# Kernel optimization log

Measured on AMD Instinct MI355X. Metric: run time of the kernel, lower is better.

Reference implementation:

```python
import jax, jax.numpy as jnp
import numpy as np

IN_F = 2048
OUT_F = 2048
BS = 64  # block_size
NIB = IN_F // BS   # 32 in-blocks
NOB = OUT_F // BS  # 32 out-blocks


def setup_inputs() -> dict:
    key = jax.random.key(0)
    k_x, k_s1, k_s2, k_m = jax.random.split(key, 4)
    bound = 1.0 / np.sqrt(BS)
    x = jax.random.normal(k_x, (4, 4096, IN_F), dtype=jnp.float32)
    stage1 = jax.random.uniform(k_s1, (NIB * BS, BS), minval=-bound, maxval=bound, dtype=jnp.float32)
    stage2 = jax.random.uniform(k_s2, (NOB * BS, BS), minval=-bound, maxval=bound, dtype=jnp.float32)
    mix_w = jax.random.normal(k_m, (NOB * BS, NIB * BS), dtype=jnp.float32) / np.sqrt(IN_F)
    return {"x": x, "stage1": stage1, "stage2": stage2, "mix_w": mix_w}


def _blockdiag(x, weight, num_blocks):
    # x: [..., num_blocks*BS]; weight: [num_blocks*BS, BS] viewed as [g, c, d]
    shape = x.shape[:-1]
    xg = x.reshape(-1, num_blocks, BS)
    w = weight.reshape(num_blocks, BS, BS)
    y = jnp.einsum('ngc,gcd->ngd', xg, w)
    return y.reshape(*shape, num_blocks * BS)


def _shuffle(x):
    # interpret last dim as [BS, NIB], transpose to [NIB, BS]
    shape = x.shape[:-1]
    return x.reshape(-1, BS, NIB).transpose(0, 2, 1).reshape(*shape, NIB * BS)


def reference(x, stage1, stage2, mix_w):
    h = _blockdiag(x, stage1, NIB)          # [B,S,IN_F]
    h = _shuffle(h)                          # [B,S,IN_F]
    h = jnp.einsum('bsi,oi->bso', h, mix_w)  # dense mix, no bias
    return _blockdiag(h, stage2, NOB)        # [B,S,OUT_F]
```

## Files before the change

### kernel.cpp

```cpp
#include <hip/hip_runtime.h>
#include <stdint.h>

#define IN_F 2048
#define OUT_F 2048
#define MTOK 16384

typedef __attribute__((ext_vector_type(8))) __bf16 bf16x8;
typedef __attribute__((ext_vector_type(4))) float f32x4;
typedef __attribute__((ext_vector_type(4))) unsigned short us4;
typedef __attribute__((ext_vector_type(8))) unsigned short us8;

typedef const __attribute__((address_space(1))) void g_void;
typedef __attribute__((address_space(3))) void l_void;

__device__ __forceinline__ void async16(void* lds, const void* g) {
    __builtin_amdgcn_global_load_lds((g_void*)(uintptr_t)g, (l_void*)(uintptr_t)lds, 16, 0, 0);
}

__device__ __forceinline__ unsigned short f2bf(float x) {
    union { float f; uint32_t u; } v; v.f = x;
    uint32_t r = v.u + 0x7fffu + ((v.u >> 16) & 1u);
    return (unsigned short)(r >> 16);
}

__device__ __forceinline__ bf16x8 f8_to_bf8(const float* __restrict__ p) {
    float4 a = *(const float4*)p;
    float4 b = *(const float4*)(p + 4);
    union { us8 u; bf16x8 h; } r;
    r.u[0] = f2bf(a.x); r.u[1] = f2bf(a.y); r.u[2] = f2bf(a.z); r.u[3] = f2bf(a.w);
    r.u[4] = f2bf(b.x); r.u[5] = f2bf(b.y); r.u[6] = f2bf(b.z); r.u[7] = f2bf(b.w);
    return r.h;
}

__global__ void k_prep(const float* __restrict__ W,
                       const float* __restrict__ s1, const float* __restrict__ s2,
                       unsigned short* __restrict__ Bp,
                       unsigned short* __restrict__ W1T, unsigned short* __restrict__ W2T) {
    __shared__ float buf[64 * 65];
    const int t = threadIdx.x;
    if (blockIdx.x < 2048) {
        const float* src = W + (size_t)blockIdx.x * IN_F;
#pragma unroll
        for (int q = 0; q < 2; ++q) {
            int id4 = q * 256 + t;
            float4 v = *(const float4*)(src + id4 * 4);
            int i = id4 * 4;
            int b = i + (i >> 5);
            buf[b] = v.x; buf[b + 1] = v.y; buf[b + 2] = v.z; buf[b + 3] = v.w;
        }
        __syncthreads();
        unsigned short* dst = Bp + (size_t)blockIdx.x * IN_F;
#pragma unroll
        for (int q = 0; q < 8; ++q) {
            int j = q * 256 + t;
            int i = ((j & 31) << 6) | (j >> 5);
            dst[j] = f2bf(buf[i + (i >> 5)]);
        }
    } else {
        const int b = blockIdx.x - 2048;
        const float* src = (b < 32 ? s1 : s2) + (size_t)(b & 31) * 4096;
        unsigned short* dst = (b < 32 ? W1T : W2T) + (size_t)(b & 31) * 4096;
#pragma unroll
        for (int q = 0; q < 16; ++q) {
            int id = q * 256 + t;
            buf[(id >> 6) * 65 + (id & 63)] = src[id];
        }
        __syncthreads();
#pragma unroll
        for (int q = 0; q < 16; ++q) {
            int id = q * 256 + t;
            int d = id >> 6, c = id & 63;
            dst[id] = f2bf(buf[c * 65 + d]);
        }
    }
}

#define HS_LD 72
__global__ __launch_bounds__(256, 4) void k_stage1(
    const float* __restrict__ X, const unsigned short* __restrict__ W1T,
    unsigned short* __restrict__ H) {
    __shared__ unsigned short Hs[128 * HS_LD];
    const int t = threadIdx.x;
    const int lane = t & 63, wave = t >> 6;
    const int quad = lane >> 4, l16 = lane & 15;
    const int m0 = blockIdx.x * 128;
    const int g = blockIdx.y;

    const unsigned short* Wg = W1T + g * 4096;
    bf16x8 wf[4][2];
#pragma unroll
    for (int j = 0; j < 4; ++j)
#pragma unroll
        for (int ks = 0; ks < 2; ++ks)
            wf[j][ks] = *(const bf16x8*)(Wg + (j * 16 + l16) * 64 + ks * 32 + quad * 8);

    bf16x8 af[2][2];
#pragma unroll
    for (int i = 0; i < 2; ++i)
#pragma unroll
        for (int ks = 0; ks < 2; ++ks)
            af[i][ks] = f8_to_bf8(X + (size_t)(m0 + wave * 32 + i * 16 + l16) * IN_F
                                    + g * 64 + ks * 32 + quad * 8);

    f32x4 acc[2][4];
#pragma unroll
    for (int i = 0; i < 2; ++i)
#pragma unroll
        for (int j = 0; j < 4; ++j) acc[i][j] = (f32x4)0.f;

#pragma unroll
    for (int ks = 0; ks < 2; ++ks)
#pragma unroll
        for (int i = 0; i < 2; ++i)
#pragma unroll
            for (int j = 0; j < 4; ++j)
                acc[i][j] = __builtin_amdgcn_mfma_f32_16x16x32_bf16(af[i][ks], wf[j][ks], acc[i][j], 0, 0, 0);

#pragma unroll
    for (int i = 0; i < 2; ++i)
#pragma unroll
        for (int j = 0; j < 4; ++j)
#pragma unroll
            for (int r = 0; r < 4; ++r)
                Hs[(wave * 32 + i * 16 + quad * 4 + r) * HS_LD + j * 16 + l16] = f2bf(acc[i][j][r]);
    __syncthreads();
#pragma unroll
    for (int p = 0; p < 4; ++p) {
        int id = p * 256 + t;
        int r = id >> 3, c = id & 7;
        us8 v = *(const us8*)(Hs + r * HS_LD + c * 8);
        *(us8*)(H + (size_t)(m0 + r) * IN_F + g * 64 + c * 8) = v;
    }
}

__global__ __launch_bounds__(256, 2) void k_mix_gemm(
    const unsigned short* __restrict__ A, const unsigned short* __restrict__ B,
    const unsigned short* __restrict__ W2T, float* __restrict__ C) {
    __shared__ unsigned short smem[16384];
    unsigned short* As = smem;
    unsigned short* Bs = smem + 8192;
    const int t = threadIdx.x;
    const int lane = t & 63, wave = t >> 6;
    const int quad = lane >> 4, l16 = lane & 15;
    const int mw = wave & 1, nw = wave >> 1;
    const int lin = blockIdx.y * 128 + blockIdx.x;
    const int m0 = (lin >> 4) * 128;
    const int n0 = (lin & 15) * 128;
    const int rr = t >> 3, chunk = t & 7;
    const int gsw = (chunk ^ (rr & 7)) * 8;
    const int lsw = l16 & 7;

    f32x4 acc[4][4];
#pragma unroll
    for (int i = 0; i < 4; ++i)
#pragma unroll
        for (int j = 0; j < 4; ++j) acc[i][j] = (f32x4)0.f;

    for (int kb = 0; kb < IN_F; kb += 64) {
#pragma unroll
        for (int q = 0; q < 4; ++q) {
            int r = q * 32 + rr;
            async16((char*)As + (size_t)(q * 4096 + t * 16),
                    A + (size_t)(m0 + r) * IN_F + kb + gsw);
            async16((char*)Bs + (size_t)(q * 4096 + t * 16),
                    B + (size_t)(n0 + r) * IN_F + kb + gsw);
        }
        __syncthreads();
#pragma unroll
        for (int ks = 0; ks < 2; ++ks) {
            bf16x8 af[4], bfr[4];
#pragma unroll
            for (int i = 0; i < 4; ++i)
                af[i] = *(const bf16x8*)(As + (mw * 64 + i * 16 + l16) * 64
                                            + (((ks * 4 + quad) ^ lsw) * 8));
#pragma unroll
            for (int j = 0; j < 4; ++j)
                bfr[j] = *(const bf16x8*)(Bs + (nw * 64 + j * 16 + l16) * 64
                                             + (((ks * 4 + quad) ^ lsw) * 8));
#pragma unroll
            for (int i = 0; i < 4; ++i)
#pragma unroll
                for (int j = 0; j < 4; ++j)
                    acc[i][j] = __builtin_amdgcn_mfma_f32_16x16x32_bf16(af[i], bfr[j], acc[i][j], 0, 0, 0);
        }
        __syncthreads();
    }

    unsigned short* P = smem + wave * 4096;
#pragma unroll
    for (int i = 0; i < 4; ++i)
#pragma unroll
        for (int j = 0; j < 4; ++j) {
            int cc = j * 2 + (l16 >> 3);
            int ci = l16 & 7;
#pragma unroll
            for (int r = 0; r < 4; ++r) {
                int pr = i * 16 + quad * 4 + r;
                P[pr * 64 + ((cc ^ (pr & 7)) * 8) + ci] = f2bf(acc[i][j][r]);
            }
        }

    const int g = (n0 >> 6) + nw;
    const unsigned short* W2g = W2T + g * 4096;
    bf16x8 wb[4][2];
#pragma unroll
    for (int j = 0; j < 4; ++j)
#pragma unroll
        for (int ks = 0; ks < 2; ++ks)
            wb[j][ks] = *(const bf16x8*)(W2g + (j * 16 + l16) * 64 + ks * 32 + quad * 8);

#pragma unroll
    for (int i = 0; i < 4; ++i) {
        bf16x8 pa0 = *(const bf16x8*)(P + (i * 16 + l16) * 64 + ((quad ^ lsw) * 8));
        bf16x8 pa1 = *(const bf16x8*)(P + (i * 16 + l16) * 64 + (((4 + quad) ^ lsw) * 8));
#pragma unroll
        for (int j = 0; j < 4; ++j) {
            f32x4 o = (f32x4)0.f;
            o = __builtin_amdgcn_mfma_f32_16x16x32_bf16(pa0, wb[j][0], o, 0, 0, 0);
            o = __builtin_amdgcn_mfma_f32_16x16x32_bf16(pa1, wb[j][1], o, 0, 0, 0);
            float* Cp = C + (size_t)(m0 + mw * 64 + i * 16 + quad * 4) * OUT_F
                          + (n0 + nw * 64 + j * 16 + l16);
#pragma unroll
            for (int r = 0; r < 4; ++r) Cp[(size_t)r * OUT_F] = o[r];
        }
    }
}

extern "C" void kernel_launch(void* const* d_in, const int* in_sizes, int n_in,
                              void* d_out, int out_size, void* d_ws, size_t ws_size,
                              hipStream_t stream) {
    const float* x  = (const float*)d_in[0];
    const float* s1 = (const float*)d_in[1];
    const float* s2 = (const float*)d_in[2];
    const float* mw = (const float*)d_in[3];
    float* out = (float*)d_out;

    char* ws = (char*)d_ws;
    unsigned short* hA  = (unsigned short*)ws;
    unsigned short* Bp  = (unsigned short*)(ws + (size_t)MTOK * IN_F * 2);
    unsigned short* W1T = (unsigned short*)(ws + (size_t)MTOK * IN_F * 2
                                               + (size_t)OUT_F * IN_F * 2);
    unsigned short* W2T = W1T + 32 * 4096;

    k_prep<<<2112, 256, 0, stream>>>(mw, s1, s2, Bp, W1T, W2T);
    k_stage1<<<dim3(128, 32), 256, 0, stream>>>(x, W1T, hA);
    k_mix_gemm<<<dim3(128, 16), 256, 0, stream>>>(hA, Bp, W2T, out);
}
```

Measured before the change: 392.7 us.

## Fold block-diagonal stages and shuffle into the dense mix weight

Since the whole pipeline is linear, both block-diagonal weights and the shuffle permutation are folded into the mix matrix, computed per call in fp32 in a prep kernel. The main GEMM then runs on bf16-converted x directly with a plain epilogue, which removes the stage-1 kernel, the intermediate H round trip and the per-tile stage-2 MFMAs. The cost is an fp32 weight-folding computation each call, plus a slightly different rounding path because x is converted to bf16 before any multiply.

```diff
diff --git a/kernel.cpp b/kernel.cpp
--- a/kernel.cpp
+++ b/kernel.cpp
@@ -8,7 +8,6 @@
 typedef __attribute__((ext_vector_type(8))) __bf16 bf16x8;
 typedef __attribute__((ext_vector_type(4))) float f32x4;
 typedef __attribute__((ext_vector_type(4))) unsigned short us4;
-typedef __attribute__((ext_vector_type(8))) unsigned short us8;
 
 typedef const __attribute__((address_space(1))) void g_void;
 typedef __attribute__((address_space(3))) void l_void;
@@ -23,119 +22,117 @@
     return (unsigned short)(r >> 16);
 }
 
-__device__ __forceinline__ bf16x8 f8_to_bf8(const float* __restrict__ p) {
-    float4 a = *(const float4*)p;
-    float4 b = *(const float4*)(p + 4);
-    union { us8 u; bf16x8 h; } r;
-    r.u[0] = f2bf(a.x); r.u[1] = f2bf(a.y); r.u[2] = f2bf(a.z); r.u[3] = f2bf(a.w);
-    r.u[4] = f2bf(b.x); r.u[5] = f2bf(b.y); r.u[6] = f2bf(b.z); r.u[7] = f2bf(b.w);
-    return r.h;
-}
-
-__global__ void k_prep(const float* __restrict__ W,
-                       const float* __restrict__ s1, const float* __restrict__ s2,
-                       unsigned short* __restrict__ Bp,
-                       unsigned short* __restrict__ W1T, unsigned short* __restrict__ W2T) {
-    __shared__ float buf[64 * 65];
+#define FP 68
+
+__global__ __launch_bounds__(256) void k_fold_conv(
+    const float* __restrict__ X, const float* __restrict__ s1,
+    const float* __restrict__ s2, const float* __restrict__ MW,
+    unsigned short* __restrict__ Xb, unsigned short* __restrict__ Bb) {
+    __shared__ float lds[3 * 64 * FP];
     const int t = threadIdx.x;
-    if (blockIdx.x < 2048) {
-        const float* src = W + (size_t)blockIdx.x * IN_F;
-#pragma unroll
-        for (int q = 0; q < 2; ++q) {
-            int id4 = q * 256 + t;
-            float4 v = *(const float4*)(src + id4 * 4);
-            int i = id4 * 4;
-            int b = i + (i >> 5);
-            buf[b] = v.x; buf[b + 1] = v.y; buf[b + 2] = v.z; buf[b + 3] = v.w;
-        }
-        __syncthreads();
-        unsigned short* dst = Bp + (size_t)blockIdx.x * IN_F;
-#pragma unroll
-        for (int q = 0; q < 8; ++q) {
-            int j = q * 256 + t;
-            int i = ((j & 31) << 6) | (j >> 5);
-            dst[j] = f2bf(buf[i + (i >> 5)]);
-        }
-    } else {
-        const int b = blockIdx.x - 2048;
-        const float* src = (b < 32 ? s1 : s2) + (size_t)(b & 31) * 4096;
-        unsigned short* dst = (b < 32 ? W1T : W2T) + (size_t)(b & 31) * 4096;
-#pragma unroll
-        for (int q = 0; q < 16; ++q) {
-            int id = q * 256 + t;
-            buf[(id >> 6) * 65 + (id & 63)] = src[id];
-        }
-        __syncthreads();
-#pragma unroll
-        for (int q = 0; q < 16; ++q) {
-            int id = q * 256 + t;
-            int d = id >> 6, c = id & 63;
-            dst[id] = f2bf(buf[c * 65 + d]);
-        }
-    }
-}
-
-#define HS_LD 72
-__global__ __launch_bounds__(256, 4) void k_stage1(
-    const float* __restrict__ X, const unsigned short* __restrict__ W1T,
-    unsigned short* __restrict__ H) {
-    __shared__ unsigned short Hs[128 * HS_LD];
-    const int t = threadIdx.x;
-    const int lane = t & 63, wave = t >> 6;
-    const int quad = lane >> 4, l16 = lane & 15;
-    const int m0 = blockIdx.x * 128;
-    const int g = blockIdx.y;
-
-    const unsigned short* Wg = W1T + g * 4096;
-    bf16x8 wf[4][2];
-#pragma unroll
-    for (int j = 0; j < 4; ++j)
-#pragma unroll
-        for (int ks = 0; ks < 2; ++ks)
-            wf[j][ks] = *(const bf16x8*)(Wg + (j * 16 + l16) * 64 + ks * 32 + quad * 8);
-
-    bf16x8 af[2][2];
-#pragma unroll
-    for (int i = 0; i < 2; ++i)
-#pragma unroll
-        for (int ks = 0; ks < 2; ++ks)
-            af[i][ks] = f8_to_bf8(X + (size_t)(m0 + wave * 32 + i * 16 + l16) * IN_F
-                                    + g * 64 + ks * 32 + quad * 8);
-
-    f32x4 acc[2][4];
-#pragma unroll
-    for (int i = 0; i < 2; ++i)
-#pragma unroll
-        for (int j = 0; j < 4; ++j) acc[i][j] = (f32x4)0.f;
-
-#pragma unroll
-    for (int ks = 0; ks < 2; ++ks)
-#pragma unroll
-        for (int i = 0; i < 2; ++i)
+    const int bx = blockIdx.x;
+
+    if (bx >= 1024) {
+        const int gid = (bx - 1024) * 256 + t;
+        const float4* src = (const float4*)X;
+        us4* dst = (us4*)Xb;
+#pragma unroll
+        for (int k = 0; k < 16; ++k) {
+            int idx = k * (2048 * 256) + gid;
+            float4 v = src[idx];
+            us4 o;
+            o[0] = f2bf(v.x); o[1] = f2bf(v.y); o[2] = f2bf(v.z); o[3] = f2bf(v.w);
+            dst[idx] = o;
+        }
+        return;
+    }
+
+    float* Wl  = lds;
+    float* Bpl = lds + 64 * FP;
+    float* M1t = lds + 128 * FP;
+    const int g  = bx & 31;
+    const int rt = bx >> 5;
+
+#pragma unroll
+    for (int q = 0; q < 4; ++q) {
+        int id = q * 256 + t;
+        int c = id >> 4, d4 = id & 15;
+        float4 v = *(const float4*)(s1 + (size_t)(g * 64 + c) * 64 + d4 * 4);
+        *(float4*)&Wl[c * FP + d4 * 4] = v;
+    }
+#pragma unroll
+    for (int q = 0; q < 8; ++q) {
+        int id = q * 256 + t;
+        int o = id >> 5, b = id & 31;
+        float2 v = *(const float2*)(MW + (size_t)(rt * 64 + o) * 2048 + b * 64 + g * 2);
+        Bpl[o * FP + b]      = v.x;
+        Bpl[o * FP + b + 32] = v.y;
+    }
+    __syncthreads();
+
+    {
+        const int co = (t & 15) * 4, oo = (t >> 4) * 4;
+        float acc[4][4] = {};
+#pragma unroll
+        for (int dc = 0; dc < 16; ++dc) {
+            float4 bv[4], wv[4];
+#pragma unroll
+            for (int i = 0; i < 4; ++i) bv[i] = *(const float4*)&Bpl[(oo + i) * FP + dc * 4];
+#pragma unroll
+            for (int j = 0; j < 4; ++j) wv[j] = *(const float4*)&Wl[(co + j) * FP + dc * 4];
+#pragma unroll
+            for (int i = 0; i < 4; ++i)
+#pragma unroll
+                for (int j = 0; j < 4; ++j)
+                    acc[i][j] += bv[i].x * wv[j].x + bv[i].y * wv[j].y
+                               + bv[i].z * wv[j].z + bv[i].w * wv[j].w;
+        }
+#pragma unroll
+        for (int i = 0; i < 4; ++i)
 #pragma unroll
             for (int j = 0; j < 4; ++j)
-                acc[i][j] = __builtin_amdgcn_mfma_f32_16x16x32_bf16(af[i][ks], wf[j][ks], acc[i][j], 0, 0, 0);
-
-#pragma unroll
-    for (int i = 0; i < 2; ++i)
-#pragma unroll
-        for (int j = 0; j < 4; ++j)
-#pragma unroll
-            for (int r = 0; r < 4; ++r)
-                Hs[(wave * 32 + i * 16 + quad * 4 + r) * HS_LD + j * 16 + l16] = f2bf(acc[i][j][r]);
+                M1t[(co + j) * FP + oo + i] = acc[i][j];
+    }
     __syncthreads();
-#pragma unroll
-    for (int p = 0; p < 4; ++p) {
-        int id = p * 256 + t;
-        int r = id >> 3, c = id & 7;
-        us8 v = *(const us8*)(Hs + r * HS_LD + c * 8);
-        *(us8*)(H + (size_t)(m0 + r) * IN_F + g * 64 + c * 8) = v;
-    }
-}
-
-__global__ __launch_bounds__(256, 2) void k_mix_gemm(
+
+#pragma unroll
+    for (int q = 0; q < 16; ++q) {
+        int id = q * 256 + t;
+        int d2 = id & 63, c2 = id >> 6;
+        Wl[d2 * FP + c2] = s2[(size_t)(rt * 64 + c2) * 64 + d2];
+    }
+    __syncthreads();
+
+    {
+        const int cco = (t & 15) * 4, d2o = (t >> 4) * 4;
+        float acc[4][4] = {};
+#pragma unroll
+        for (int kc = 0; kc < 16; ++kc) {
+            float4 wv[4], mv[4];
+#pragma unroll
+            for (int i = 0; i < 4; ++i) wv[i] = *(const float4*)&Wl[(d2o + i) * FP + kc * 4];
+#pragma unroll
+            for (int j = 0; j < 4; ++j) mv[j] = *(const float4*)&M1t[(cco + j) * FP + kc * 4];
+#pragma unroll
+            for (int i = 0; i < 4; ++i)
+#pragma unroll
+                for (int j = 0; j < 4; ++j)
+                    acc[i][j] += wv[i].x * mv[j].x + wv[i].y * mv[j].y
+                               + wv[i].z * mv[j].z + wv[i].w * mv[j].w;
+        }
+#pragma unroll
+        for (int i = 0; i < 4; ++i) {
+            us4 o;
+            o[0] = f2bf(acc[i][0]); o[1] = f2bf(acc[i][1]);
+            o[2] = f2bf(acc[i][2]); o[3] = f2bf(acc[i][3]);
+            *(us4*)(Bb + (size_t)(rt * 64 + d2o + i) * 2048 + g * 64 + cco) = o;
+        }
+    }
+}
+
+__global__ __launch_bounds__(256, 2) void k_gemm(
     const unsigned short* __restrict__ A, const unsigned short* __restrict__ B,
-    const unsigned short* __restrict__ W2T, float* __restrict__ C) {
+    float* __restrict__ C) {
     __shared__ unsigned short smem[16384];
     unsigned short* As = smem;
     unsigned short* Bs = smem + 8192;
@@ -186,44 +183,15 @@
         __syncthreads();
     }
 
-    unsigned short* P = smem + wave * 4096;
 #pragma unroll
     for (int i = 0; i < 4; ++i)
 #pragma unroll
         for (int j = 0; j < 4; ++j) {
-            int cc = j * 2 + (l16 >> 3);
-            int ci = l16 & 7;
-#pragma unroll
-            for (int r = 0; r < 4; ++r) {
-                int pr = i * 16 + quad * 4 + r;
-                P[pr * 64 + ((cc ^ (pr & 7)) * 8) + ci] = f2bf(acc[i][j][r]);
-            }
-        }
-
-    const int g = (n0 >> 6) + nw;
-    const unsigned short* W2g = W2T + g * 4096;
-    bf16x8 wb[4][2];
-#pragma unroll
-    for (int j = 0; j < 4; ++j)
-#pragma unroll
-        for (int ks = 0; ks < 2; ++ks)
-            wb[j][ks] = *(const bf16x8*)(W2g + (j * 16 + l16) * 64 + ks * 32 + quad * 8);
-
-#pragma unroll
-    for (int i = 0; i < 4; ++i) {
-        bf16x8 pa0 = *(const bf16x8*)(P + (i * 16 + l16) * 64 + ((quad ^ lsw) * 8));
-        bf16x8 pa1 = *(const bf16x8*)(P + (i * 16 + l16) * 64 + (((4 + quad) ^ lsw) * 8));
-#pragma unroll
-        for (int j = 0; j < 4; ++j) {
-            f32x4 o = (f32x4)0.f;
-            o = __builtin_amdgcn_mfma_f32_16x16x32_bf16(pa0, wb[j][0], o, 0, 0, 0);
-            o = __builtin_amdgcn_mfma_f32_16x16x32_bf16(pa1, wb[j][1], o, 0, 0, 0);
             float* Cp = C + (size_t)(m0 + mw * 64 + i * 16 + quad * 4) * OUT_F
                           + (n0 + nw * 64 + j * 16 + l16);
 #pragma unroll
-            for (int r = 0; r < 4; ++r) Cp[(size_t)r * OUT_F] = o[r];
-        }
-    }
+            for (int r = 0; r < 4; ++r) Cp[(size_t)r * OUT_F] = acc[i][j][r];
+        }
 }
 
 extern "C" void kernel_launch(void* const* d_in, const int* in_sizes, int n_in,
@@ -236,13 +204,9 @@
     float* out = (float*)d_out;
 
     char* ws = (char*)d_ws;
-    unsigned short* hA  = (unsigned short*)ws;
-    unsigned short* Bp  = (unsigned short*)(ws + (size_t)MTOK * IN_F * 2);
-    unsigned short* W1T = (unsigned short*)(ws + (size_t)MTOK * IN_F * 2
-                                               + (size_t)OUT_F * IN_F * 2);
-    unsigned short* W2T = W1T + 32 * 4096;
-
-    k_prep<<<2112, 256, 0, stream>>>(mw, s1, s2, Bp, W1T, W2T);
-    k_stage1<<<dim3(128, 32), 256, 0, stream>>>(x, W1T, hA);
-    k_mix_gemm<<<dim3(128, 16), 256, 0, stream>>>(hA, Bp, W2T, out);
-}
+    unsigned short* Xb = (unsigned short*)ws;
+    unsigned short* Bb = (unsigned short*)(ws + (size_t)MTOK * IN_F * 2);
+
+    k_fold_conv<<<3072, 256, 0, stream>>>(x, s1, s2, mw, Xb, Bb);
+    k_gemm<<<dim3(128, 16), 256, 0, stream>>>(Xb, Bb, out);
+}
```

After: 468.3 us. +19.3%, slower.
